# Performance work log

Hardware: AMD Instinct MI355X
Metric: run time of the kernel (lower is better)

Reference implementation:

```python
import jax, jax.numpy as jnp
import numpy as np

HIDDEN = 1024
QKV = 1024
HEADS = 16
HEAD_DIM = QKV // HEADS
B, S = 4, 4096


def setup_inputs() -> dict:
    key = jax.random.key(0)
    ks = jax.random.split(key, 8)
    s = 1.0 / np.sqrt(HIDDEN)
    return {
        "x": jax.random.normal(ks[0], (B, S, HIDDEN), dtype=jnp.float32),
        "mask": jnp.ones((B, S, 1), dtype=jnp.float32),
        "Wq": jax.random.uniform(ks[1], (HIDDEN, QKV), jnp.float32, -s, s),
        "bq": jax.random.uniform(ks[2], (QKV,), jnp.float32, -s, s),
        "Wk": jax.random.uniform(ks[3], (HIDDEN, QKV), jnp.float32, -s, s),
        "bk": jax.random.uniform(ks[4], (QKV,), jnp.float32, -s, s),
        "Wv": jax.random.uniform(ks[5], (HIDDEN, QKV), jnp.float32, -s, s),
        "bv": jax.random.uniform(ks[6], (QKV,), jnp.float32, -s, s),
    }


def _split_heads(t):
    # [B, S, QKV] -> [B, H, S, D]
    b, s, _ = t.shape
    return t.reshape(b, s, HEADS, HEAD_DIM).transpose(0, 2, 1, 3)


def reference(x, mask, Wq, bq, Wk, bk, Wv, bv):
    q = (x @ Wq + bq) * mask  # [B, S, QKV]
    k = (x @ Wk + bk) * mask
    v = (x @ Wv + bv) * mask
    q, k, v = _split_heads(q), _split_heads(k), _split_heads(v)  # [B,H,S,D]
    # k^T @ v : [B, H, D, D]
    kv = jnp.einsum('bhsd,bhse->bhde', k, v)
    # per-batch norm constant from mask sum
    norm = mask.sum(axis=(-1, -2))  # [B]
    norm = 1.0 / jnp.sqrt(norm * HEAD_DIM)
    kv = kv * norm[:, None, None, None]
    # dropout is identity in eval mode
    out = jnp.einsum('bhsd,bhde->bhse', q, kv)  # [B, H, S, D]
    out = out.transpose(0, 2, 1, 3).reshape(B, S, QKV)
    return out
```

## Files before the change

### kernel.cpp

```cpp
#include <hip/hip_runtime.h>
#include <stdint.h>

#define HIDDEN 1024
#define SEQ 4096
#define BATCH 4
#define HEADS 16
#define HDIM 64
#define M_TOT (BATCH * SEQ)
#define NCH 4
#define NT64 16

typedef __bf16 bf16x8 __attribute__((ext_vector_type(8)));
typedef float f32x4 __attribute__((ext_vector_type(4)));
typedef unsigned short u16x8 __attribute__((ext_vector_type(8)));

static __device__ __forceinline__ unsigned short f2bf(float f) {
  union { float f; uint32_t u; } v; v.f = f;
  uint32_t u = v.u;
  uint32_t r = (u + 0x7fffu + ((u >> 16) & 1u)) >> 16;
  return (unsigned short)r;
}
static __device__ __forceinline__ void load_lds16(const void* g, void* l) {
  __builtin_amdgcn_global_load_lds(
      (__attribute__((address_space(1))) void*)(g),
      (__attribute__((address_space(3))) void*)(l), 16, 0, 0);
}

__global__ __launch_bounds__(256) void prep_k(
    const float* __restrict__ x, unsigned short* __restrict__ xb,
    const float* __restrict__ Wk, const float* __restrict__ Wv,
    unsigned short* __restrict__ Bt,
    const float* __restrict__ bk, const float* __restrict__ bv,
    float* __restrict__ bkv,
    const float* __restrict__ mask, float* __restrict__ norm) {
  const int bid = blockIdx.x;
  const int tid = threadIdx.x;
  __shared__ float ts[64][65];
  if (bid < 8192) {
    int idx = bid * 256 + tid;
    const float4* xv = (const float4*)x;
    float4 a = xv[(size_t)idx * 2];
    float4 b = xv[(size_t)idx * 2 + 1];
    u16x8 o;
    o[0] = f2bf(a.x); o[1] = f2bf(a.y); o[2] = f2bf(a.z); o[3] = f2bf(a.w);
    o[4] = f2bf(b.x); o[5] = f2bf(b.y); o[6] = f2bf(b.z); o[7] = f2bf(b.w);
    *(u16x8*)(xb + (size_t)idx * 8) = o;
  } else if (bid < 8704) {
    int idx = bid - 8192;
    int z = idx >> 8, rem = idx & 255;
    const float* W = z ? Wv : Wk;
    unsigned short* out = Bt + (size_t)z * HIDDEN * HIDDEN;
    int n0 = (rem & 15) * 64, k0 = (rem >> 4) * 64;
    int c = tid & 63, rq = tid >> 6;
    for (int i = 0; i < 16; ++i) {
      int r = i * 4 + rq;
      ts[r][c] = W[(size_t)(k0 + r) * HIDDEN + n0 + c];
    }
    __syncthreads();
    for (int i = 0; i < 16; ++i) {
      int n = i * 4 + rq;
      out[(size_t)(n0 + n) * HIDDEN + k0 + c] = f2bf(ts[c][n]);
    }
  } else if (bid < 8712) {
    int i = (bid - 8704) * 256 + tid;
    bkv[i] = (i < HIDDEN) ? bk[i] : bv[i - HIDDEN];
  } else {
    int b = bid - 8712;
    float s = 0.f;
    for (int i = tid; i < SEQ; i += 256) s += mask[b * SEQ + i];
    for (int off = 32; off; off >>= 1) s += __shfl_down(s, off);
    __shared__ float wsum[4];
    if ((tid & 63) == 0) wsum[tid >> 6] = s;
    __syncthreads();
    if (tid == 0) {
      float t = wsum[0] + wsum[1] + wsum[2] + wsum[3];
      norm[b] = rsqrtf(t * (float)HDIM);
    }
  }
}

template <int OUT_MODE, int PER_BATCH_B>
__global__ __launch_bounds__(512, 2) void gemm256_k(
    const unsigned short* __restrict__ A, const unsigned short* __restrict__ Bt,
    const float* __restrict__ bias, const float* __restrict__ mask,
    void* __restrict__ C, int ldc, int nbn) {
  __shared__ unsigned short smem[65536];

  const int nwg = gridDim.x;
  const int bid = blockIdx.x;
  const int wg = (bid & 7) * (nwg >> 3) + (bid >> 3);
  const int row0 = (wg / nbn) * 256;
  const int col0 = (wg % nbn) * 256;

  const unsigned short* Bbase = Bt;
  const float* biasbase = bias;
  if (PER_BATCH_B) {
    int b = row0 >> 12;
    Bbase = Bt + (size_t)b * HIDDEN * HIDDEN;
    biasbase = bias + b * HIDDEN;
  }

  const int tid = threadIdx.x;
  const int wave = tid >> 6;
  const int lane = tid & 63;
  const int wm = wave >> 2;
  const int wn = wave & 3;
  const int lr = lane & 15;
  const int hi = lane >> 4;

  const int srow = tid >> 3;
  const int scol = ((tid & 7) ^ (srow & 7)) * 8;
  const unsigned short* sA = A + (size_t)(row0 + srow) * HIDDEN + scol;
  const unsigned short* sB = Bbase + (size_t)(col0 + srow) * HIDDEN + scol;
  const int ldst = tid * 8;

#define STAGE(half, tt, isB) { \
    int dst_ = ((tt)&1) * 32768 + (isB) * 16384 + (half) * 8192 + ldst; \
    const unsigned short* src_ = ((isB) ? sB : sA) + (size_t)(half) * 128 * HIDDEN + (tt) * 64; \
    load_lds16(src_, &smem[dst_]); \
    load_lds16(src_ + (size_t)64 * HIDDEN, &smem[dst_ + 4096]); }

  const int chunk0 = (hi ^ (lr & 7)) * 8;
  const int chunk1 = ((4 + hi) ^ (lr & 7)) * 8;
  const int arow = (wm * 128 + lr) * 64;
  const int brow = 16384 + (wn * 64 + lr) * 64;

  f32x4 acc[8][4];
#pragma unroll
  for (int i = 0; i < 8; ++i)
#pragma unroll
    for (int j = 0; j < 4; ++j) acc[i][j] = (f32x4){0.f, 0.f, 0.f, 0.f};

  STAGE(0, 0, 0) STAGE(1, 0, 0) STAGE(0, 0, 1) STAGE(1, 0, 1)
  STAGE(0, 1, 1) STAGE(1, 1, 1)
  asm volatile("s_waitcnt vmcnt(4)" ::: "memory");
  __builtin_amdgcn_s_barrier();

  bf16x8 af[4][2], b0f[2][2], b1f[2][2];
  for (int t = 0; t < NT64; ++t) {
    const int bb = (t & 1) * 32768;
#pragma unroll
    for (int rf = 0; rf < 4; ++rf) {
      af[rf][0] = *(const bf16x8*)&smem[bb + arow + rf * 1024 + chunk0];
      af[rf][1] = *(const bf16x8*)&smem[bb + arow + rf * 1024 + chunk1];
    }
#pragma unroll
    for (int cf = 0; cf < 2; ++cf) {
      b0f[cf][0] = *(const bf16x8*)&smem[bb + brow + cf * 1024 + chunk0];
      b0f[cf][1] = *(const bf16x8*)&smem[bb + brow + cf * 1024 + chunk1];
    }
    if (t + 1 < NT64) STAGE(0, t + 1, 0)
    __builtin_amdgcn_s_setprio(1);
#pragma unroll
    for (int rf = 0; rf < 4; ++rf)
#pragma unroll
      for (int cf = 0; cf < 2; ++cf)
#pragma unroll
        for (int kh = 0; kh < 2; ++kh)
          acc[rf][cf] = __builtin_amdgcn_mfma_f32_16x16x32_bf16(af[rf][kh], b0f[cf][kh], acc[rf][cf], 0, 0, 0);
    __builtin_amdgcn_s_setprio(0);
    asm volatile("" ::: "memory");
    __builtin_amdgcn_s_barrier();
#pragma unroll
    for (int cf = 0; cf < 2; ++cf) {
      b1f[cf][0] = *(const bf16x8*)&smem[bb + brow + 2048 + cf * 1024 + chunk0];
      b1f[cf][1] = *(const bf16x8*)&smem[bb + brow + 2048 + cf * 1024 + chunk1];
    }
    if (t + 1 < NT64) STAGE(1, t + 1, 0)
    __builtin_amdgcn_s_setprio(1);
#pragma unroll
    for (int rf = 0; rf < 4; ++rf)
#pragma unroll
      for (int cf = 0; cf < 2; ++cf)
#pragma unroll
        for (int kh = 0; kh < 2; ++kh)
          acc[rf][2 + cf] = __builtin_amdgcn_mfma_f32_16x16x32_bf16(af[rf][kh], b1f[cf][kh], acc[rf][2 + cf], 0, 0, 0);
    __builtin_amdgcn_s_setprio(0);
    asm volatile("" ::: "memory");
    __builtin_amdgcn_s_barrier();
#pragma unroll
    for (int rf = 0; rf < 4; ++rf) {
      af[rf][0] = *(const bf16x8*)&smem[bb + arow + 4096 + rf * 1024 + chunk0];
      af[rf][1] = *(const bf16x8*)&smem[bb + arow + 4096 + rf * 1024 + chunk1];
    }
    __builtin_amdgcn_s_setprio(1);
#pragma unroll
    for (int rf = 0; rf < 4; ++rf)
#pragma unroll
      for (int cf = 0; cf < 2; ++cf)
#pragma unroll
        for (int kh = 0; kh < 2; ++kh)
          acc[4 + rf][cf] = __builtin_amdgcn_mfma_f32_16x16x32_bf16(af[rf][kh], b0f[cf][kh], acc[4 + rf][cf], 0, 0, 0);
    __builtin_amdgcn_s_setprio(0);
    asm volatile("" ::: "memory");
    __builtin_amdgcn_s_barrier();
    if (t + 2 < NT64) { STAGE(0, t + 2, 1) STAGE(1, t + 2, 1) }
    __builtin_amdgcn_s_setprio(1);
#pragma unroll
    for (int rf = 0; rf < 4; ++rf)
#pragma unroll
      for (int cf = 0; cf < 2; ++cf)
#pragma unroll
        for (int kh = 0; kh < 2; ++kh)
          acc[4 + rf][2 + cf] = __builtin_amdgcn_mfma_f32_16x16x32_bf16(af[rf][kh], b1f[cf][kh], acc[4 + rf][2 + cf], 0, 0, 0);
    __builtin_amdgcn_s_setprio(0);
    if (t < NT64 - 3) asm volatile("s_waitcnt vmcnt(4)" ::: "memory");
    else              asm volatile("s_waitcnt vmcnt(0)" ::: "memory");
    __builtin_amdgcn_s_barrier();
  }

  float bcol[4];
#pragma unroll
  for (int an = 0; an < 4; ++an)
    bcol[an] = biasbase[col0 + wn * 64 + (an >> 1) * 32 + (an & 1) * 16 + lr];

  if (OUT_MODE == 2) {
    const int b = row0 >> 12;
    const int s0 = (row0 & 4095) + wm * 128;
    unsigned short* wt = &smem[wave * 4096];
    unsigned short* KVt = (unsigned short*)C;
#pragma unroll
    for (int half = 0; half < 2; ++half) {
#pragma unroll
      for (int am4 = 0; am4 < 4; ++am4) {
#pragma unroll
        for (int j = 0; j < 4; ++j) {
          int r = am4 * 16 + hi * 4 + j;
          float mrow = mask[row0 + wm * 128 + half * 64 + r];
#pragma unroll
          for (int an = 0; an < 4; ++an) {
            int c = (an >> 1) * 32 + (an & 1) * 16 + lr;
            wt[c * 64 + (r ^ ((c & 7) << 3))] =
                f2bf((acc[half * 4 + am4][an][j] + bcol[an]) * mrow);
          }
        }
      }
      asm volatile("s_waitcnt lgkmcnt(0)" ::: "memory");
#pragma unroll
      for (int i = 0; i < 8; ++i) {
        int flat = i * 64 + lane;
        int c = flat >> 3, rq = flat & 7;
        uint4 vv = *(const uint4*)&wt[c * 64 + ((rq * 8) ^ ((c & 7) << 3))];
        *(uint4*)&KVt[((size_t)(col0 + wn * 64 + c) * 4 + b) * 4096 + s0 + half * 64 + rq * 8] = vv;
      }
      asm volatile("s_waitcnt lgkmcnt(0)" ::: "memory");
    }
  } else {
    float* wf = (float*)&smem[(size_t)wave * 8192];
    float* Cg = (float*)C;
#pragma unroll
    for (int h = 0; h < 2; ++h) {
#pragma unroll
      for (int am4 = 0; am4 < 4; ++am4) {
        int am = h * 4 + am4;
#pragma unroll
        for (int j = 0; j < 4; ++j) {
          int r = am4 * 16 + hi * 4 + j;
          float mrow = mask[row0 + wm * 128 + h * 64 + r];
#pragma unroll
          for (int an = 0; an < 4; ++an) {
            int c = (an >> 1) * 32 + (an & 1) * 16 + lr;
            wf[r * 64 + c] = (acc[am][an][j] + bcol[an]) * mrow;
          }
        }
      }
      asm volatile("s_waitcnt lgkmcnt(0)" ::: "memory");
#pragma unroll
      for (int i = 0; i < 16; ++i) {
        int e4 = i * 64 + lane;
        int r = e4 >> 4, c4 = e4 & 15;
        *(float4*)&Cg[(size_t)(row0 + wm * 128 + h * 64 + r) * ldc + col0 + wn * 64 + c4 * 4] =
            *(const float4*)&wf[r * 64 + c4 * 4];
      }
      asm volatile("s_waitcnt lgkmcnt(0)" ::: "memory");
    }
  }
#undef STAGE
}

__global__ __launch_bounds__(256) void kvpart2_k(const unsigned short* __restrict__ KVt,
                                                 float* __restrict__ part) {
  const int bh = blockIdx.x, ch = blockIdx.y;
  const int b = bh >> 4, h = bh & 15;
  __shared__ unsigned short tl[32768];
  const int tid = threadIdx.x;
  const int wave = tid >> 6, lane = tid & 63;
  const int lr = lane & 15, hi = lane >> 4;

  const int r0 = tid >> 3;
  const int cc0 = ((tid & 7) ^ (r0 & 7)) * 8;
  const int r1 = 32 + r0;
  const int cc1 = ((tid & 7) ^ (r1 & 7)) * 8;
  const unsigned short* A0 = KVt + ((size_t)(h * 64 + r0) * 4 + b) * 4096 + ch * 1024 + cc0;
  const unsigned short* A1 = KVt + ((size_t)(h * 64 + r1) * 4 + b) * 4096 + ch * 1024 + cc1;
  const unsigned short* B0 = KVt + ((size_t)(1024 + h * 64 + r0) * 4 + b) * 4096 + ch * 1024 + cc0;
  const unsigned short* B1 = KVt + ((size_t)(1024 + h * 64 + r1) * 4 + b) * 4096 + ch * 1024 + cc1;

#define KSTAGE(tt) { int bb2 = ((tt) & 3) * 8192; \
    load_lds16(A0 + (tt) * 64, &tl[bb2 + tid * 8]); \
    load_lds16(A1 + (tt) * 64, &tl[bb2 + 2048 + tid * 8]); \
    load_lds16(B0 + (tt) * 64, &tl[bb2 + 4096 + tid * 8]); \
    load_lds16(B1 + (tt) * 64, &tl[bb2 + 6144 + tid * 8]); }

  const int ra = wave * 16 + lr;
  const int aoff = ra * 64;
  const int ach0 = (hi ^ (ra & 7)) * 8, ach1 = ((4 + hi) ^ (ra & 7)) * 8;

  f32x4 acc4[4];
#pragma unroll
  for (int nt = 0; nt < 4; ++nt) acc4[nt] = (f32x4){0.f, 0.f, 0.f, 0.f};

  KSTAGE(0) KSTAGE(1)
  asm volatile("s_waitcnt vmcnt(4)" ::: "memory");
  __builtin_amdgcn_s_barrier();
  for (int t = 0; t < 16; ++t) {
    const int bb = (t & 3) * 8192;
    if (t + 2 < 16) KSTAGE(t + 2)
    bf16x8 a0 = *(const bf16x8*)&tl[bb + aoff + ach0];
    bf16x8 a1 = *(const bf16x8*)&tl[bb + aoff + ach1];
    bf16x8 bf0[4], bf1[4];
#pragma unroll
    for (int nt = 0; nt < 4; ++nt) {
      int rb = nt * 16 + lr;
      bf0[nt] = *(const bf16x8*)&tl[bb + 4096 + rb * 64 + ((hi ^ (rb & 7)) * 8)];
      bf1[nt] = *(const bf16x8*)&tl[bb + 4096 + rb * 64 + (((4 + hi) ^ (rb & 7)) * 8)];
    }
#pragma unroll
    for (int nt = 0; nt < 4; ++nt) {
      acc4[nt] = __builtin_amdgcn_mfma_f32_16x16x32_bf16(a0, bf0[nt], acc4[nt], 0, 0, 0);
      acc4[nt] = __builtin_amdgcn_mfma_f32_16x16x32_bf16(a1, bf1[nt], acc4[nt], 0, 0, 0);
    }
    if (t < 14) asm volatile("s_waitcnt vmcnt(4)" ::: "memory");
    else        asm volatile("s_waitcnt vmcnt(0)" ::: "memory");
    __builtin_amdgcn_s_barrier();
  }
  float* dst = part + ((size_t)ch * 64 + bh) * 4096;
#pragma unroll
  for (int nt = 0; nt < 4; ++nt)
#pragma unroll
    for (int j = 0; j < 4; ++j)
      dst[(wave * 16 + hi * 4 + j) * 64 + nt * 16 + lr] = acc4[nt][j];
#undef KSTAGE
}

__global__ void kvreduce_k(const float* __restrict__ part, const float* __restrict__ norm,
                           float* __restrict__ kv) {
  int idx = blockIdx.x * 256 + threadIdx.x;
  int b = idx >> 16;
  float s = 0.f;
#pragma unroll
  for (int ch = 0; ch < NCH; ++ch) s += part[(size_t)ch * 262144 + idx];
  kv[idx] = s * norm[b];
}

__global__ void bias2_k(const float* __restrict__ bq, const float* __restrict__ kv,
                        float* __restrict__ bias2) {
  int idx = blockIdx.x * 256 + threadIdx.x;
  int b = idx >> 10, n = idx & 1023, h = n >> 6, e = n & 63;
  const float* kvp = kv + ((size_t)(b * 16 + h)) * 4096 + e;
  float s = 0.f;
#pragma unroll
  for (int d = 0; d < 64; ++d) s += bq[h * 64 + d] * kvp[d * 64];
  bias2[idx] = s;
}

__global__ __launch_bounds__(128) void wprime_k(const float* __restrict__ Wq,
                                                const float* __restrict__ kv,
                                                unsigned short* __restrict__ Wpt) {
  int bh = blockIdx.y, b = bh >> 4, h = bh & 15;
  int c0 = blockIdx.x * 128;
  __shared__ float wqs[128][65];
  __shared__ float kvs[64][64];
  int tid = threadIdx.x;
  for (int i = 0; i < 32; ++i) {
    int idx = i * 128 + tid;
    ((float*)kvs)[idx] = kv[(size_t)bh * 4096 + idx];
  }
  int rr = tid >> 6, cc = tid & 63;
  for (int i = 0; i < 64; ++i) {
    int r = i * 2 + rr;
    wqs[r][cc] = Wq[(size_t)(c0 + r) * HIDDEN + h * 64 + cc];
  }
  __syncthreads();
  float acc[64];
#pragma unroll
  for (int e = 0; e < 64; ++e) acc[e] = 0.f;
  for (int d = 0; d < 64; ++d) {
    float w = wqs[tid][d];
#pragma unroll
    for (int e4 = 0; e4 < 64; e4 += 4) {
      f32x4 kvv = *(const f32x4*)&kvs[d][e4];
      acc[e4 + 0] += w * kvv[0];
      acc[e4 + 1] += w * kvv[1];
      acc[e4 + 2] += w * kvv[2];
      acc[e4 + 3] += w * kvv[3];
    }
  }
  unsigned short* dst = Wpt + (size_t)b * HIDDEN * HIDDEN + (size_t)(h * 64) * HIDDEN + (c0 + tid);
#pragma unroll
  for (int e = 0; e < 64; ++e) dst[(size_t)e * HIDDEN] = f2bf(acc[e]);
}

extern "C" void kernel_launch(void* const* d_in, const int* in_sizes, int n_in,
                              void* d_out, int out_size, void* d_ws, size_t ws_size,
                              hipStream_t stream) {
  const float* x = (const float*)d_in[0];
  const float* mask = (const float*)d_in[1];
  const float* Wq = (const float*)d_in[2];
  const float* bq = (const float*)d_in[3];
  const float* Wk = (const float*)d_in[4];
  const float* bk = (const float*)d_in[5];
  const float* Wv = (const float*)d_in[6];
  const float* bv = (const float*)d_in[7];
  float* out = (float*)d_out;

  char* w = (char*)d_ws;
  unsigned short* xb = (unsigned short*)w;  w += (size_t)M_TOT * HIDDEN * 2;
  unsigned short* Bt = (unsigned short*)w;  w += (size_t)2048 * HIDDEN * 2;
  unsigned short* KVt = (unsigned short*)w; w += (size_t)2048 * BATCH * SEQ * 2;
  float* part = (float*)w;                  w += (size_t)NCH * 64 * 4096 * 4;
  float* kv = (float*)w;                    w += (size_t)64 * 4096 * 4;
  unsigned short* Wpt = (unsigned short*)w; w += (size_t)BATCH * HIDDEN * HIDDEN * 2;
  float* bkv = (float*)w;                   w += 2048 * 4;
  float* bias2 = (float*)w;                 w += 4096 * 4;
  float* norm = (float*)w;                  w += 64;

  prep_k<<<dim3(8716), dim3(256), 0, stream>>>(x, xb, Wk, Wv, Bt, bk, bv, bkv, mask, norm);
  gemm256_k<2, 0><<<dim3(512), dim3(512), 0, stream>>>(xb, Bt, bkv, mask, (void*)KVt, 0, 8);
  kvpart2_k<<<dim3(64, NCH), dim3(256), 0, stream>>>(KVt, part);
  kvreduce_k<<<dim3(1024), dim3(256), 0, stream>>>(part, norm, kv);
  bias2_k<<<dim3(16), dim3(256), 0, stream>>>(bq, kv, bias2);
  wprime_k<<<dim3(8, 64), dim3(128), 0, stream>>>(Wq, kv, Wpt);
  gemm256_k<0, 1><<<dim3(256), dim3(512), 0, stream>>>(xb, Wpt, bias2, mask, (void*)out, 1024, 4);
}
```

Measured before the change: 168.6 us.

## Reschedule GEMM main loop with sched barriers and split staging; store output directly

```diff
diff --git a/kernel.cpp b/kernel.cpp
--- a/kernel.cpp
+++ b/kernel.cpp
@@ -133,8 +133,20 @@
 
   STAGE(0, 0, 0) STAGE(1, 0, 0) STAGE(0, 0, 1) STAGE(1, 0, 1)
   STAGE(0, 1, 1) STAGE(1, 1, 1)
-  asm volatile("s_waitcnt vmcnt(4)" ::: "memory");
+  asm volatile("s_waitcnt vmcnt(4)");
   __builtin_amdgcn_s_barrier();
+
+#define MFMA16(AMBASE, BF) \
+  { __builtin_amdgcn_s_setprio(1); \
+    _Pragma("unroll") \
+    for (int rf = 0; rf < 4; ++rf) \
+      _Pragma("unroll") \
+      for (int cf = 0; cf < 2; ++cf) \
+        _Pragma("unroll") \
+        for (int kh = 0; kh < 2; ++kh) \
+          acc[(AMBASE) + rf][((BF) ? 2 : 0) + cf] = __builtin_amdgcn_mfma_f32_16x16x32_bf16( \
+              af[rf][kh], ((BF) ? b1f : b0f)[cf][kh], acc[(AMBASE) + rf][((BF) ? 2 : 0) + cf], 0, 0, 0); \
+    __builtin_amdgcn_s_setprio(0); }
 
   bf16x8 af[4][2], b0f[2][2], b1f[2][2];
   for (int t = 0; t < NT64; ++t) {
@@ -150,16 +162,13 @@
       b0f[cf][1] = *(const bf16x8*)&smem[bb + brow + cf * 1024 + chunk1];
     }
     if (t + 1 < NT64) STAGE(0, t + 1, 0)
-    __builtin_amdgcn_s_setprio(1);
-#pragma unroll
-    for (int rf = 0; rf < 4; ++rf)
-#pragma unroll
-      for (int cf = 0; cf < 2; ++cf)
-#pragma unroll
-        for (int kh = 0; kh < 2; ++kh)
-          acc[rf][cf] = __builtin_amdgcn_mfma_f32_16x16x32_bf16(af[rf][kh], b0f[cf][kh], acc[rf][cf], 0, 0, 0);
-    __builtin_amdgcn_s_setprio(0);
-    asm volatile("" ::: "memory");
+    __builtin_amdgcn_sched_barrier(0);
+    asm volatile("s_waitcnt lgkmcnt(8)");
+    __builtin_amdgcn_s_barrier();
+    asm volatile("s_waitcnt lgkmcnt(0)");
+    __builtin_amdgcn_sched_barrier(0);
+    MFMA16(0, 0)
+    __builtin_amdgcn_sched_barrier(0);
     __builtin_amdgcn_s_barrier();
 #pragma unroll
     for (int cf = 0; cf < 2; ++cf) {
@@ -167,47 +176,36 @@
       b1f[cf][1] = *(const bf16x8*)&smem[bb + brow + 2048 + cf * 1024 + chunk1];
     }
     if (t + 1 < NT64) STAGE(1, t + 1, 0)
-    __builtin_amdgcn_s_setprio(1);
-#pragma unroll
-    for (int rf = 0; rf < 4; ++rf)
-#pragma unroll
-      for (int cf = 0; cf < 2; ++cf)
-#pragma unroll
-        for (int kh = 0; kh < 2; ++kh)
-          acc[rf][2 + cf] = __builtin_amdgcn_mfma_f32_16x16x32_bf16(af[rf][kh], b1f[cf][kh], acc[rf][2 + cf], 0, 0, 0);
-    __builtin_amdgcn_s_setprio(0);
-    asm volatile("" ::: "memory");
+    __builtin_amdgcn_sched_barrier(0);
+    __builtin_amdgcn_s_barrier();
+    asm volatile("s_waitcnt lgkmcnt(0)");
+    __builtin_amdgcn_sched_barrier(0);
+    MFMA16(0, 1)
+    __builtin_amdgcn_sched_barrier(0);
     __builtin_amdgcn_s_barrier();
 #pragma unroll
     for (int rf = 0; rf < 4; ++rf) {
       af[rf][0] = *(const bf16x8*)&smem[bb + arow + 4096 + rf * 1024 + chunk0];
       af[rf][1] = *(const bf16x8*)&smem[bb + arow + 4096 + rf * 1024 + chunk1];
     }
-    __builtin_amdgcn_s_setprio(1);
-#pragma unroll
-    for (int rf = 0; rf < 4; ++rf)
-#pragma unroll
-      for (int cf = 0; cf < 2; ++cf)
-#pragma unroll
-        for (int kh = 0; kh < 2; ++kh)
-          acc[4 + rf][cf] = __builtin_amdgcn_mfma_f32_16x16x32_bf16(af[rf][kh], b0f[cf][kh], acc[4 + rf][cf], 0, 0, 0);
-    __builtin_amdgcn_s_setprio(0);
-    asm volatile("" ::: "memory");
-    __builtin_amdgcn_s_barrier();
-    if (t + 2 < NT64) { STAGE(0, t + 2, 1) STAGE(1, t + 2, 1) }
-    __builtin_amdgcn_s_setprio(1);
-#pragma unroll
-    for (int rf = 0; rf < 4; ++rf)
-#pragma unroll
-      for (int cf = 0; cf < 2; ++cf)
-#pragma unroll
-        for (int kh = 0; kh < 2; ++kh)
-          acc[4 + rf][2 + cf] = __builtin_amdgcn_mfma_f32_16x16x32_bf16(af[rf][kh], b1f[cf][kh], acc[4 + rf][2 + cf], 0, 0, 0);
-    __builtin_amdgcn_s_setprio(0);
-    if (t < NT64 - 3) asm volatile("s_waitcnt vmcnt(4)" ::: "memory");
-    else              asm volatile("s_waitcnt vmcnt(0)" ::: "memory");
-    __builtin_amdgcn_s_barrier();
-  }
+    if (t + 2 < NT64) STAGE(0, t + 2, 1)
+    __builtin_amdgcn_sched_barrier(0);
+    __builtin_amdgcn_s_barrier();
+    asm volatile("s_waitcnt lgkmcnt(0)");
+    __builtin_amdgcn_sched_barrier(0);
+    MFMA16(4, 0)
+    __builtin_amdgcn_sched_barrier(0);
+    __builtin_amdgcn_s_barrier();
+    if (t + 2 < NT64) STAGE(1, t + 2, 1)
+    __builtin_amdgcn_sched_barrier(0);
+    __builtin_amdgcn_s_barrier();
+    MFMA16(4, 1)
+    __builtin_amdgcn_sched_barrier(0);
+    if (t < NT64 - 2) asm volatile("s_waitcnt vmcnt(4)");
+    else              asm volatile("s_waitcnt vmcnt(0)");
+    __builtin_amdgcn_s_barrier();
+  }
+#undef MFMA16
 
   float bcol[4];
 #pragma unroll
@@ -246,33 +244,22 @@
       asm volatile("s_waitcnt lgkmcnt(0)" ::: "memory");
     }
   } else {
-    float* wf = (float*)&smem[(size_t)wave * 8192];
     float* Cg = (float*)C;
 #pragma unroll
-    for (int h = 0; h < 2; ++h) {
-#pragma unroll
-      for (int am4 = 0; am4 < 4; ++am4) {
-        int am = h * 4 + am4;
-#pragma unroll
-        for (int j = 0; j < 4; ++j) {
-          int r = am4 * 16 + hi * 4 + j;
-          float mrow = mask[row0 + wm * 128 + h * 64 + r];
-#pragma unroll
-          for (int an = 0; an < 4; ++an) {
-            int c = (an >> 1) * 32 + (an & 1) * 16 + lr;
-            wf[r * 64 + c] = (acc[am][an][j] + bcol[an]) * mrow;
-          }
+    for (int am = 0; am < 8; ++am) {
+      int rbase = (am >> 2) * 64 + (am & 3) * 16 + hi * 4;
+#pragma unroll
+      for (int j = 0; j < 4; ++j) {
+        int r = rbase + j;
+        float mrow = mask[row0 + wm * 128 + r];
+#pragma unroll
+        for (int an = 0; an < 4; ++an) {
+          int c = (an >> 1) * 32 + (an & 1) * 16 + lr;
+          __builtin_nontemporal_store(
+              (acc[am][an][j] + bcol[an]) * mrow,
+              &Cg[(size_t)(row0 + wm * 128 + r) * ldc + col0 + wn * 64 + c]);
         }
       }
-      asm volatile("s_waitcnt lgkmcnt(0)" ::: "memory");
-#pragma unroll
-      for (int i = 0; i < 16; ++i) {
-        int e4 = i * 64 + lane;
-        int r = e4 >> 4, c4 = e4 & 15;
-        *(float4*)&Cg[(size_t)(row0 + wm * 128 + h * 64 + r) * ldc + col0 + wn * 64 + c4 * 4] =
-            *(const float4*)&wf[r * 64 + c4 * 4];
-      }
-      asm volatile("s_waitcnt lgkmcnt(0)" ::: "memory");
     }
   }
 #undef STAGE
```

Result: slower. 173.9 us (+3.2%).

## Compute Q explicitly and apply KV per head instead of folding into Wq

Applied to the files above, without the earlier changes.

```diff
diff --git a/kernel.cpp b/kernel.cpp
--- a/kernel.cpp
+++ b/kernel.cpp
@@ -29,7 +29,8 @@
 __global__ __launch_bounds__(256) void prep_k(
     const float* __restrict__ x, unsigned short* __restrict__ xb,
     const float* __restrict__ Wk, const float* __restrict__ Wv,
-    unsigned short* __restrict__ Bt,
+    const float* __restrict__ Wq,
+    unsigned short* __restrict__ Bt, unsigned short* __restrict__ Wqt,
     const float* __restrict__ bk, const float* __restrict__ bv,
     float* __restrict__ bkv,
     const float* __restrict__ mask, float* __restrict__ norm) {
@@ -45,11 +46,11 @@
     o[0] = f2bf(a.x); o[1] = f2bf(a.y); o[2] = f2bf(a.z); o[3] = f2bf(a.w);
     o[4] = f2bf(b.x); o[5] = f2bf(b.y); o[6] = f2bf(b.z); o[7] = f2bf(b.w);
     *(u16x8*)(xb + (size_t)idx * 8) = o;
-  } else if (bid < 8704) {
+  } else if (bid < 8960) {
     int idx = bid - 8192;
     int z = idx >> 8, rem = idx & 255;
-    const float* W = z ? Wv : Wk;
-    unsigned short* out = Bt + (size_t)z * HIDDEN * HIDDEN;
+    const float* W = (z == 0) ? Wk : (z == 1) ? Wv : Wq;
+    unsigned short* out = (z == 2) ? Wqt : (Bt + (size_t)z * HIDDEN * HIDDEN);
     int n0 = (rem & 15) * 64, k0 = (rem >> 4) * 64;
     int c = tid & 63, rq = tid >> 6;
     for (int i = 0; i < 16; ++i) {
@@ -61,11 +62,11 @@
       int n = i * 4 + rq;
       out[(size_t)(n0 + n) * HIDDEN + k0 + c] = f2bf(ts[c][n]);
     }
-  } else if (bid < 8712) {
-    int i = (bid - 8704) * 256 + tid;
+  } else if (bid < 8968) {
+    int i = (bid - 8960) * 256 + tid;
     bkv[i] = (i < HIDDEN) ? bk[i] : bv[i - HIDDEN];
   } else {
-    int b = bid - 8712;
+    int b = bid - 8968;
     float s = 0.f;
     for (int i = tid; i < SEQ; i += 256) s += mask[b * SEQ + i];
     for (int off = 32; off; off >>= 1) s += __shfl_down(s, off);
@@ -79,11 +80,11 @@
   }
 }
 
-template <int OUT_MODE, int PER_BATCH_B>
+template <int OUT_MODE>
 __global__ __launch_bounds__(512, 2) void gemm256_k(
     const unsigned short* __restrict__ A, const unsigned short* __restrict__ Bt,
     const float* __restrict__ bias, const float* __restrict__ mask,
-    void* __restrict__ C, int ldc, int nbn) {
+    void* __restrict__ C, int nbn) {
   __shared__ unsigned short smem[65536];
 
   const int nwg = gridDim.x;
@@ -91,14 +92,6 @@
   const int wg = (bid & 7) * (nwg >> 3) + (bid >> 3);
   const int row0 = (wg / nbn) * 256;
   const int col0 = (wg % nbn) * 256;
-
-  const unsigned short* Bbase = Bt;
-  const float* biasbase = bias;
-  if (PER_BATCH_B) {
-    int b = row0 >> 12;
-    Bbase = Bt + (size_t)b * HIDDEN * HIDDEN;
-    biasbase = bias + b * HIDDEN;
-  }
 
   const int tid = threadIdx.x;
   const int wave = tid >> 6;
@@ -111,7 +104,7 @@
   const int srow = tid >> 3;
   const int scol = ((tid & 7) ^ (srow & 7)) * 8;
   const unsigned short* sA = A + (size_t)(row0 + srow) * HIDDEN + scol;
-  const unsigned short* sB = Bbase + (size_t)(col0 + srow) * HIDDEN + scol;
+  const unsigned short* sB = Bt + (size_t)(col0 + srow) * HIDDEN + scol;
   const int ldst = tid * 8;
 
 #define STAGE(half, tt, isB) { \
@@ -212,7 +205,7 @@
   float bcol[4];
 #pragma unroll
   for (int an = 0; an < 4; ++an)
-    bcol[an] = biasbase[col0 + wn * 64 + (an >> 1) * 32 + (an & 1) * 16 + lr];
+    bcol[an] = bias[col0 + wn * 64 + (an >> 1) * 32 + (an & 1) * 16 + lr];
 
   if (OUT_MODE == 2) {
     const int b = row0 >> 12;
@@ -246,31 +239,31 @@
       asm volatile("s_waitcnt lgkmcnt(0)" ::: "memory");
     }
   } else {
-    float* wf = (float*)&smem[(size_t)wave * 8192];
-    float* Cg = (float*)C;
-#pragma unroll
-    for (int h = 0; h < 2; ++h) {
+    unsigned short* qv = (unsigned short*)C;
+    unsigned short* wt = &smem[wave * 4096];
+#pragma unroll
+    for (int half = 0; half < 2; ++half) {
 #pragma unroll
       for (int am4 = 0; am4 < 4; ++am4) {
-        int am = h * 4 + am4;
 #pragma unroll
         for (int j = 0; j < 4; ++j) {
           int r = am4 * 16 + hi * 4 + j;
-          float mrow = mask[row0 + wm * 128 + h * 64 + r];
+          float mrow = mask[row0 + wm * 128 + half * 64 + r];
 #pragma unroll
           for (int an = 0; an < 4; ++an) {
             int c = (an >> 1) * 32 + (an & 1) * 16 + lr;
-            wf[r * 64 + c] = (acc[am][an][j] + bcol[an]) * mrow;
+            wt[r * 64 + (c ^ ((r & 7) << 3))] =
+                f2bf((acc[half * 4 + am4][an][j] + bcol[an]) * mrow);
           }
         }
       }
       asm volatile("s_waitcnt lgkmcnt(0)" ::: "memory");
 #pragma unroll
-      for (int i = 0; i < 16; ++i) {
-        int e4 = i * 64 + lane;
-        int r = e4 >> 4, c4 = e4 & 15;
-        *(float4*)&Cg[(size_t)(row0 + wm * 128 + h * 64 + r) * ldc + col0 + wn * 64 + c4 * 4] =
-            *(const float4*)&wf[r * 64 + c4 * 4];
+      for (int i = 0; i < 8; ++i) {
+        int flat = i * 512 + lane * 8;
+        int r = flat >> 6, c0 = flat & 63;
+        uint4 vv = *(const uint4*)&wt[r * 64 + (c0 ^ ((r & 7) << 3))];
+        *(uint4*)&qv[(size_t)(row0 + wm * 128 + half * 64 + r) * 1024 + col0 + wn * 64 + c0] = vv;
       }
       asm volatile("s_waitcnt lgkmcnt(0)" ::: "memory");
     }
@@ -334,7 +327,7 @@
     else        asm volatile("s_waitcnt vmcnt(0)" ::: "memory");
     __builtin_amdgcn_s_barrier();
   }
-  float* dst = part + ((size_t)ch * 64 + bh) * 4096;
+  float* dst = part + ((size_t)(ch * 64 + bh)) * 4096;
 #pragma unroll
   for (int nt = 0; nt < 4; ++nt)
 #pragma unroll
@@ -344,61 +337,55 @@
 }
 
 __global__ void kvreduce_k(const float* __restrict__ part, const float* __restrict__ norm,
-                           float* __restrict__ kv) {
-  int idx = blockIdx.x * 256 + threadIdx.x;
-  int b = idx >> 16;
-  float s = 0.f;
-#pragma unroll
-  for (int ch = 0; ch < NCH; ++ch) s += part[(size_t)ch * 262144 + idx];
-  kv[idx] = s * norm[b];
-}
-
-__global__ void bias2_k(const float* __restrict__ bq, const float* __restrict__ kv,
-                        float* __restrict__ bias2) {
-  int idx = blockIdx.x * 256 + threadIdx.x;
-  int b = idx >> 10, n = idx & 1023, h = n >> 6, e = n & 63;
-  const float* kvp = kv + ((size_t)(b * 16 + h)) * 4096 + e;
-  float s = 0.f;
-#pragma unroll
-  for (int d = 0; d < 64; ++d) s += bq[h * 64 + d] * kvp[d * 64];
-  bias2[idx] = s;
-}
-
-__global__ __launch_bounds__(128) void wprime_k(const float* __restrict__ Wq,
-                                                const float* __restrict__ kv,
-                                                unsigned short* __restrict__ Wpt) {
-  int bh = blockIdx.y, b = bh >> 4, h = bh & 15;
-  int c0 = blockIdx.x * 128;
-  __shared__ float wqs[128][65];
-  __shared__ float kvs[64][64];
-  int tid = threadIdx.x;
-  for (int i = 0; i < 32; ++i) {
-    int idx = i * 128 + tid;
-    ((float*)kvs)[idx] = kv[(size_t)bh * 4096 + idx];
-  }
-  int rr = tid >> 6, cc = tid & 63;
-  for (int i = 0; i < 64; ++i) {
-    int r = i * 2 + rr;
-    wqs[r][cc] = Wq[(size_t)(c0 + r) * HIDDEN + h * 64 + cc];
-  }
-  __syncthreads();
-  float acc[64];
-#pragma unroll
-  for (int e = 0; e < 64; ++e) acc[e] = 0.f;
-  for (int d = 0; d < 64; ++d) {
-    float w = wqs[tid][d];
-#pragma unroll
-    for (int e4 = 0; e4 < 64; e4 += 4) {
-      f32x4 kvv = *(const f32x4*)&kvs[d][e4];
-      acc[e4 + 0] += w * kvv[0];
-      acc[e4 + 1] += w * kvv[1];
-      acc[e4 + 2] += w * kvv[2];
-      acc[e4 + 3] += w * kvv[3];
-    }
-  }
-  unsigned short* dst = Wpt + (size_t)b * HIDDEN * HIDDEN + (size_t)(h * 64) * HIDDEN + (c0 + tid);
-#pragma unroll
-  for (int e = 0; e < 64; ++e) dst[(size_t)e * HIDDEN] = f2bf(acc[e]);
+                           unsigned short* __restrict__ kvt) {
+  int idx4 = (blockIdx.x * 256 + threadIdx.x) * 4;
+  int bh = idx4 >> 12, rem = idx4 & 4095;
+  int e = rem >> 6, d0 = rem & 63;
+  float s0 = 0.f, s1 = 0.f, s2 = 0.f, s3 = 0.f;
+#pragma unroll
+  for (int ch = 0; ch < NCH; ++ch) {
+    const float* p = part + ((size_t)(ch * 64 + bh)) * 4096 + e;
+    s0 += p[(d0 + 0) * 64];
+    s1 += p[(d0 + 1) * 64];
+    s2 += p[(d0 + 2) * 64];
+    s3 += p[(d0 + 3) * 64];
+  }
+  float nb = norm[bh >> 4];
+  ushort4 o;
+  o.x = f2bf(s0 * nb); o.y = f2bf(s1 * nb); o.z = f2bf(s2 * nb); o.w = f2bf(s3 * nb);
+  *(ushort4*)&kvt[idx4] = o;
+}
+
+__global__ __launch_bounds__(256) void qkv_k(const unsigned short* __restrict__ q,
+                                             const unsigned short* __restrict__ kvt,
+                                             float* __restrict__ out) {
+  const int s0 = blockIdx.x * 64;
+  const int b = s0 >> 12;
+  const int tid = threadIdx.x;
+  const int wave = tid >> 6, lane = tid & 63;
+  const int lr = lane & 15, hi = lane >> 4;
+  const unsigned short* qrow = q + (size_t)(s0 + wave * 16 + lr) * 1024;
+#pragma unroll 1
+  for (int h = 0; h < 16; ++h) {
+    const unsigned short* kvb = kvt + ((size_t)(b * 16 + h)) * 4096;
+    bf16x8 a0 = *(const bf16x8*)&qrow[h * 64 + hi * 8];
+    bf16x8 a1 = *(const bf16x8*)&qrow[h * 64 + 32 + hi * 8];
+    f32x4 acc4[4];
+#pragma unroll
+    for (int et = 0; et < 4; ++et) {
+      bf16x8 b0 = *(const bf16x8*)&kvb[(et * 16 + lr) * 64 + hi * 8];
+      bf16x8 b1 = *(const bf16x8*)&kvb[(et * 16 + lr) * 64 + 32 + hi * 8];
+      acc4[et] = (f32x4){0.f, 0.f, 0.f, 0.f};
+      acc4[et] = __builtin_amdgcn_mfma_f32_16x16x32_bf16(a0, b0, acc4[et], 0, 0, 0);
+      acc4[et] = __builtin_amdgcn_mfma_f32_16x16x32_bf16(a1, b1, acc4[et], 0, 0, 0);
+    }
+#pragma unroll
+    for (int et = 0; et < 4; ++et)
+#pragma unroll
+      for (int j = 0; j < 4; ++j)
+        __builtin_nontemporal_store(acc4[et][j],
+            &out[(size_t)(s0 + wave * 16 + hi * 4 + j) * 1024 + h * 64 + et * 16 + lr]);
+  }
 }
 
 extern "C" void kernel_launch(void* const* d_in, const int* in_sizes, int n_in,
@@ -415,21 +402,20 @@
   float* out = (float*)d_out;
 
   char* w = (char*)d_ws;
-  unsigned short* xb = (unsigned short*)w;  w += (size_t)M_TOT * HIDDEN * 2;
-  unsigned short* Bt = (unsigned short*)w;  w += (size_t)2048 * HIDDEN * 2;
-  unsigned short* KVt = (unsigned short*)w; w += (size_t)2048 * BATCH * SEQ * 2;
-  float* part = (float*)w;                  w += (size_t)NCH * 64 * 4096 * 4;
-  float* kv = (float*)w;                    w += (size_t)64 * 4096 * 4;
-  unsigned short* Wpt = (unsigned short*)w; w += (size_t)BATCH * HIDDEN * HIDDEN * 2;
-  float* bkv = (float*)w;                   w += 2048 * 4;
-  float* bias2 = (float*)w;                 w += 4096 * 4;
-  float* norm = (float*)w;                  w += 64;
-
-  prep_k<<<dim3(8716), dim3(256), 0, stream>>>(x, xb, Wk, Wv, Bt, bk, bv, bkv, mask, norm);
-  gemm256_k<2, 0><<<dim3(512), dim3(512), 0, stream>>>(xb, Bt, bkv, mask, (void*)KVt, 0, 8);
+  unsigned short* xb = (unsigned short*)w;   w += (size_t)M_TOT * HIDDEN * 2;
+  unsigned short* Bt = (unsigned short*)w;   w += (size_t)2048 * HIDDEN * 2;
+  unsigned short* Wqt = (unsigned short*)w;  w += (size_t)HIDDEN * HIDDEN * 2;
+  unsigned short* KVt = (unsigned short*)w;  w += (size_t)2048 * BATCH * SEQ * 2;
+  float* part = (float*)w;                   w += (size_t)NCH * 64 * 4096 * 4;
+  unsigned short* kvt = (unsigned short*)w;  w += (size_t)64 * 4096 * 2;
+  float* bkv = (float*)w;                    w += 2048 * 4;
+  float* norm = (float*)w;                   w += 64;
+  unsigned short* q = KVt;
+
+  prep_k<<<dim3(8972), dim3(256), 0, stream>>>(x, xb, Wk, Wv, Wq, Bt, Wqt, bk, bv, bkv, mask, norm);
+  gemm256_k<2><<<dim3(512), dim3(512), 0, stream>>>(xb, Bt, bkv, mask, (void*)KVt, 8);
   kvpart2_k<<<dim3(64, NCH), dim3(256), 0, stream>>>(KVt, part);
-  kvreduce_k<<<dim3(1024), dim3(256), 0, stream>>>(part, norm, kv);
-  bias2_k<<<dim3(16), dim3(256), 0, stream>>>(bq, kv, bias2);
-  wprime_k<<<dim3(8, 64), dim3(128), 0, stream>>>(Wq, kv, Wpt);
-  gemm256_k<0, 1><<<dim3(256), dim3(512), 0, stream>>>(xb, Wpt, bias2, mask, (void*)out, 1024, 4);
-}
+  kvreduce_k<<<dim3(256), dim3(256), 0, stream>>>(part, norm, kvt);
+  gemm256_k<3><<<dim3(256), dim3(512), 0, stream>>>(xb, Wqt, bq, mask, (void*)q, 4);
+  qkv_k<<<dim3(256), dim3(256), 0, stream>>>(q, kvt, out);
+}
```

Measured after the change: 168.9 us. About the same (+0.2%).
